# Kernel optimization log

Hardware: AMD Instinct MI355X
Metric: run time of the kernel (lower is better)

The kernel has to match this reference:

```python
import jax, jax.numpy as jnp
import numpy as np

B = 128  # number of graphs/molecules in batch


def setup_inputs() -> dict:
    key = jax.random.key(0)
    ks = jax.random.split(key, 6)
    T, C, D = 131072, 512, 512  # total nodes, feature_dim, out_dim
    hidden_states = jax.random.normal(ks[0], (T, C), dtype=jnp.float32)
    data_batch = jnp.sort(jax.random.randint(ks[1], (T,), 0, B, dtype=jnp.int32))
    lim1 = 1.0 / np.sqrt(C)
    lim2 = 1.0 / np.sqrt(D)
    return {
        "hidden_states": hidden_states,
        "data_batch": data_batch,
        "max_nodes": 1280,
        "ln_gamma": jnp.ones((C,), jnp.float32),
        "ln_beta": jnp.zeros((C,), jnp.float32),
        "W1": jax.random.uniform(ks[2], (D, C), jnp.float32, -lim1, lim1),
        "b1": jax.random.uniform(ks[3], (D,), jnp.float32, -lim1, lim1),
        "W2": jax.random.uniform(ks[4], (D, D), jnp.float32, -lim2, lim2),
        "b2": jax.random.uniform(ks[5], (D,), jnp.float32, -lim2, lim2),
    }


def reference(hidden_states, data_batch, max_nodes, ln_gamma, ln_beta, W1, b1, W2, b2):
    T, C = hidden_states.shape
    # ragged -> dense scatter: position of each node within its batch group
    counts = jnp.bincount(data_batch, length=B)               # [B]
    offsets = jnp.cumsum(counts) - counts                      # exclusive cumsum [B]
    pos = jnp.arange(T, dtype=jnp.int32) - offsets[data_batch]  # [T]
    result = jnp.zeros((B, max_nodes, C), hidden_states.dtype).at[data_batch, pos].set(hidden_states)
    # mask: a padded row is all-zero
    mask = jnp.any(result != 0, axis=-1)[..., None].astype(result.dtype)  # [B, N, 1]
    # LayerNorm (eps=1e-5, torch default)
    mu = jnp.mean(result, axis=-1, keepdims=True)
    var = jnp.mean((result - mu) ** 2, axis=-1, keepdims=True)
    logits = (result - mu) * jax.lax.rsqrt(var + 1e-5) * ln_gamma + ln_beta
    cap_embes = logits @ W1.T + b1                              # [B, N, D]
    features_in = cap_embes @ W2.T + b2                         # [B, N, D]
    features_in = jnp.where(mask == 0, -10000.0, features_in)
    attn = jax.nn.softmax(features_in, axis=1)                  # softmax over nodes
    attn = jnp.where(mask == 0, 0.0, attn)
    return jnp.sum(attn * cap_embes, axis=1)                    # [B, D]
```

## Files before the change

### kernel.cpp

```cpp
#include <hip/hip_runtime.h>
#include <hip/hip_bf16.h>


typedef short short8 __attribute__((ext_vector_type(8)));
typedef short short4v __attribute__((ext_vector_type(4)));
typedef float f32x4 __attribute__((ext_vector_type(4)));

__device__ inline short f2bf(float f) {
    unsigned u = __float_as_uint(f);
    u += 0x7fffu + ((u >> 16) & 1u);
    return (short)(u >> 16);
}

__device__ inline size_t packed_off(int n, int k) {
    const int t = n >> 4, l16n = n & 15;
    const int k0 = k >> 5, quad = (k >> 3) & 3, j = k & 7;
    return ((size_t)((t * 16 + k0) * 64 + quad * 16 + l16n)) * 8 + j;
}

#define PREP_GRID 229

__global__ __launch_bounds__(512)
void esa_prep_all(const float* __restrict__ W1, const float* __restrict__ W2,
                  const float* __restrict__ b1, const float* __restrict__ b2,
                  const int* __restrict__ db, int T, int B,
                  short* __restrict__ W1p, short* __restrict__ W12p,
                  float* __restrict__ b12, int4* __restrict__ entries, int maxent,
                  float* __restrict__ numden) {
    __shared__ int off[513];
    __shared__ int nch[512];
    __shared__ int scan[513];
    const int bid = blockIdx.x;
    const int tid = threadIdx.x;

    if (bid < 64) {
        const int ti = bid >> 3, tj = bid & 7;
        const int wave = tid >> 6;
        const int lane = tid & 63;
        const int quad = lane >> 4;
        const int l16 = lane & 15;
        const int mhalf = wave >> 2;
        const int kq = wave & 3;
        const int kcol = tj * 64 + kq * 16 + l16;

        f32x4 acc[2];
        acc[0] = (f32x4)0.0f; acc[1] = (f32x4)0.0f;
        for (int j0 = 0; j0 < 512; j0 += 32) {
            short8 bfr;
#pragma unroll
            for (int jj = 0; jj < 8; ++jj)
                bfr[jj] = f2bf(W1[(size_t)(j0 + quad * 8 + jj) * 512 + kcol]);
#pragma unroll
            for (int mt = 0; mt < 2; ++mt) {
                const float* ar = W2 + (size_t)(ti * 64 + (mhalf * 2 + mt) * 16 + l16) * 512 +
                                  j0 + quad * 8;
                const float4 a0 = *(const float4*)ar;
                const float4 a1 = *(const float4*)(ar + 4);
                short8 afr = {f2bf(a0.x), f2bf(a0.y), f2bf(a0.z), f2bf(a0.w),
                              f2bf(a1.x), f2bf(a1.y), f2bf(a1.z), f2bf(a1.w)};
                acc[mt] = __builtin_amdgcn_mfma_f32_16x16x32_bf16(afr, bfr,
                                                                  acc[mt], 0, 0, 0);
            }
        }
#pragma unroll
        for (int mt = 0; mt < 2; ++mt)
#pragma unroll
            for (int r = 0; r < 4; ++r) {
                const int n = ti * 64 + (mhalf * 2 + mt) * 16 + quad * 4 + r;
                W12p[packed_off(n, kcol)] = f2bf(acc[mt][r]);
            }
    } else if (bid < 192) {
        const int gid = (bid - 64) * 512 + tid;
        const int i4 = gid * 4;
        const int n = i4 >> 9, k = i4 & 511;
        const float4 a = *(const float4*)(W1 + i4);
        short4v sa = {f2bf(a.x), f2bf(a.y), f2bf(a.z), f2bf(a.w)};
        *(short4v*)(W1p + packed_off(n, k)) = sa;
    } else if (bid < 196) {
        const int row = (bid - 192) * 128 + (tid >> 2);
        const int part = tid & 3;
        const float* wr = W2 + (size_t)row * 512;
        float acc = 0.0f;
#pragma unroll 4
        for (int i = 0; i < 32; ++i) {
            const float4 w = *(const float4*)(wr + (i * 4 + part) * 4);
            const float4 bb = *(const float4*)(b1 + (i * 4 + part) * 4);
            acc += w.x * bb.x + w.y * bb.y + w.z * bb.z + w.w * bb.w;
        }
        acc += __shfl_xor(acc, 1);
        acc += __shfl_xor(acc, 2);
        if (part == 0) b12[row] = acc + b2[row];
    } else if (bid == 196) {
        for (int t = tid; t <= B; t += 512) {
            if (t == B) {
                off[t] = T;
            } else {
                int lo = 0, hi = T;
                while (lo < hi) {
                    int mid = (lo + hi) >> 1;
                    if (db[mid] < t) lo = mid + 1; else hi = mid;
                }
                off[t] = lo;
            }
        }
        __syncthreads();
        for (int t = tid; t < B; t += 512)
            nch[t] = (off[t + 1] - off[t] + 63) >> 6;
        __syncthreads();
        if (tid == 0) {
            int s = 0;
            for (int i = 0; i < B; ++i) { scan[i] = s; s += nch[i]; }
            scan[B] = s;
        }
        __syncthreads();
        for (int t = tid; t < B; t += 512) {
            int cnt = off[t + 1] - off[t];
            for (int j = 0; j < nch[t]; ++j) {
                int v = cnt - j * 64;
                if (v > 64) v = 64;
                entries[scan[t] + j] = make_int4(t, off[t] + j * 64, v, 0);
            }
        }
        int total = scan[B];
        for (int i = total + tid; i < maxent; i += 512)
            entries[i] = make_int4(0, 0, 0, 0);
    } else {
        const int idx = (bid - 197) * 512 + tid;
        float4 z = {0.0f, 0.0f, 0.0f, 0.0f};
        *(float4*)(numden + (size_t)idx * 8) = z;
        *(float4*)(numden + (size_t)idx * 8 + 4) = z;
    }
}

__global__ __launch_bounds__(512, 4)
void esa_fused(const float* __restrict__ x, const float* __restrict__ gamma,
               const float* __restrict__ beta, const short* __restrict__ W1p,
               const short* __restrict__ W12p, const float* __restrict__ b1,
               const float* __restrict__ b12, const int4* __restrict__ entries,
               float* __restrict__ num, float* __restrict__ den) {
    __shared__ short ylds[64 * 512];
    const int4 e = entries[blockIdx.x];
    const int bat = e.x, start = e.y, valid = e.z;
    if (valid <= 0) return;

    const int tid = threadIdx.x;
    const int wave = tid >> 6;
    const int lane = tid & 63;
    const int quad = lane >> 4;
    const int l16 = lane & 15;

    const float4 g0 = *(const float4*)(gamma + lane * 8);
    const float4 g1 = *(const float4*)(gamma + lane * 8 + 4);
    const float4 be0 = *(const float4*)(beta + lane * 8);
    const float4 be1 = *(const float4*)(beta + lane * 8 + 4);

#pragma unroll
    for (int g = 0; g < 2; ++g) {
        float4 ra[4], rb[4];
        float s[4], ss[4];
#pragma unroll
        for (int r = 0; r < 4; ++r) {
            const int m = wave * 8 + g * 4 + r;
            const int mc = m < valid ? m : valid - 1;
            const float* xr = x + (size_t)(start + mc) * 512 + lane * 8;
            ra[r] = *(const float4*)xr;
            rb[r] = *(const float4*)(xr + 4);
        }
#pragma unroll
        for (int r = 0; r < 4; ++r) {
            s[r] = ra[r].x + ra[r].y + ra[r].z + ra[r].w +
                   rb[r].x + rb[r].y + rb[r].z + rb[r].w;
            ss[r] = ra[r].x * ra[r].x + ra[r].y * ra[r].y + ra[r].z * ra[r].z +
                    ra[r].w * ra[r].w + rb[r].x * rb[r].x + rb[r].y * rb[r].y +
                    rb[r].z * rb[r].z + rb[r].w * rb[r].w;
        }
#pragma unroll
        for (int o = 1; o <= 32; o <<= 1) {
#pragma unroll
            for (int r = 0; r < 4; ++r) {
                s[r] += __shfl_xor(s[r], o);
                ss[r] += __shfl_xor(ss[r], o);
            }
        }
#pragma unroll
        for (int r = 0; r < 4; ++r) {
            const int m = wave * 8 + g * 4 + r;
            const float mu = s[r] * (1.0f / 512.0f);
            const float var = ss[r] * (1.0f / 512.0f) - mu * mu;
            const float rstd = rsqrtf(var + 1e-5f);
            short8 outv;
            outv[0] = f2bf((ra[r].x - mu) * rstd * g0.x + be0.x);
            outv[1] = f2bf((ra[r].y - mu) * rstd * g0.y + be0.y);
            outv[2] = f2bf((ra[r].z - mu) * rstd * g0.z + be0.z);
            outv[3] = f2bf((ra[r].w - mu) * rstd * g0.w + be0.w);
            outv[4] = f2bf((rb[r].x - mu) * rstd * g1.x + be1.x);
            outv[5] = f2bf((rb[r].y - mu) * rstd * g1.y + be1.y);
            outv[6] = f2bf((rb[r].z - mu) * rstd * g1.z + be1.z);
            outv[7] = f2bf((rb[r].w - mu) * rstd * g1.w + be1.w);
            *(short8*)&ylds[m * 512 + ((lane ^ (m & 7)) * 8)] = outv;
        }
    }
    __syncthreads();

    const int xr7 = l16 & 7;
    const short* abase = ylds + l16 * 512;
    const bool full = (valid >= 64);

    for (int grp = 0; grp < 2; ++grp) {
        const int n0 = wave * 64 + grp * 32;
        const int ntile0 = n0 >> 4;
        f32x4 acc_c[2][4], acc_f[2][4];
#pragma unroll
        for (int nt = 0; nt < 2; ++nt)
#pragma unroll
            for (int mt = 0; mt < 4; ++mt) {
                acc_c[nt][mt] = (f32x4)0.0f;
                acc_f[nt][mt] = (f32x4)0.0f;
            }
        const short* w1t0 = W1p + (size_t)ntile0 * 8192 + lane * 8;
        const short* w1t1 = w1t0 + 8192;
        const short* w2t0 = W12p + (size_t)ntile0 * 8192 + lane * 8;
        const short* w2t1 = w2t0 + 8192;

        short8 b10 = *(const short8*)(w1t0);
        short8 b11 = *(const short8*)(w1t1);
        short8 b20 = *(const short8*)(w2t0);
        short8 b21 = *(const short8*)(w2t1);

#pragma unroll 2
        for (int k0 = 0; k0 < 16; ++k0) {
            const int kn = (k0 + 1) & 15;
            const short8 nb10 = *(const short8*)(w1t0 + kn * 512);
            const short8 nb11 = *(const short8*)(w1t1 + kn * 512);
            const short8 nb20 = *(const short8*)(w2t0 + kn * 512);
            const short8 nb21 = *(const short8*)(w2t1 + kn * 512);

            const int blk = ((k0 << 2) | quad) ^ xr7;
            const short* ap = abase + blk * 8;

            __builtin_amdgcn_s_setprio(1);
#pragma unroll
            for (int mt = 0; mt < 4; ++mt) {
                const short8 afr = *(const short8*)(ap + mt * 16 * 512);
                acc_c[0][mt] = __builtin_amdgcn_mfma_f32_16x16x32_bf16(
                    afr, b10, acc_c[0][mt], 0, 0, 0);
                acc_c[1][mt] = __builtin_amdgcn_mfma_f32_16x16x32_bf16(
                    afr, b11, acc_c[1][mt], 0, 0, 0);
                acc_f[0][mt] = __builtin_amdgcn_mfma_f32_16x16x32_bf16(
                    afr, b20, acc_f[0][mt], 0, 0, 0);
                acc_f[1][mt] = __builtin_amdgcn_mfma_f32_16x16x32_bf16(
                    afr, b21, acc_f[1][mt], 0, 0, 0);
            }
            __builtin_amdgcn_s_setprio(0);
            b10 = nb10; b11 = nb11; b20 = nb20; b21 = nb21;
        }
#pragma unroll
        for (int nt = 0; nt < 2; ++nt) {
            const int n = n0 + nt * 16 + l16;
            const float bb1 = b1[n];
            const float bb2 = b12[n];
            float se = 0.0f, sec = 0.0f;
            if (full) {
#pragma unroll
                for (int mt = 0; mt < 4; ++mt) {
#pragma unroll
                    for (int r2 = 0; r2 < 4; ++r2) {
                        const float cap = acc_c[nt][mt][r2] + bb1;
                        const float ev = __expf(acc_f[nt][mt][r2] + bb2);
                        se += ev;
                        sec += ev * cap;
                    }
                }
            } else {
#pragma unroll
                for (int mt = 0; mt < 4; ++mt) {
#pragma unroll
                    for (int r2 = 0; r2 < 4; ++r2) {
                        const int m = mt * 16 + quad * 4 + r2;
                        if (m < valid) {
                            const float cap = acc_c[nt][mt][r2] + bb1;
                            const float ev = __expf(acc_f[nt][mt][r2] + bb2);
                            se += ev;
                            sec += ev * cap;
                        }
                    }
                }
            }
            se += __shfl_xor(se, 16);
            se += __shfl_xor(se, 32);
            sec += __shfl_xor(sec, 16);
            sec += __shfl_xor(sec, 32);
            if (quad == 0) atomicAdd(&den[(size_t)bat * 512 + n], se);
            else if (quad == 1) atomicAdd(&num[(size_t)bat * 512 + n], sec);
        }
    }
}

__global__ __launch_bounds__(256)
void esa_finalize(const float* __restrict__ num, const float* __restrict__ den,
                  float* __restrict__ out, int n) {
    const int i = blockIdx.x * 256 + threadIdx.x;
    if (i < n) {
        const float d = den[i];
        out[i] = d > 0.0f ? num[i] / d : 0.0f;
    }
}

extern "C" void kernel_launch(void* const* d_in, const int* in_sizes, int n_in,
                              void* d_out, int out_size, void* d_ws, size_t ws_size,
                              hipStream_t stream) {
    const float* x = (const float*)d_in[0];
    const int* db = (const int*)d_in[1];
    const float* gamma = (const float*)d_in[3];
    const float* beta = (const float*)d_in[4];
    const float* W1 = (const float*)d_in[5];
    const float* b1 = (const float*)d_in[6];
    const float* W2 = (const float*)d_in[7];
    const float* b2 = (const float*)d_in[8];
    float* out = (float*)d_out;

    const int C = in_sizes[3];
    const int D = in_sizes[6];
    const int T = in_sizes[0] / C;
    const int B = out_size / D;
    const int maxent = B + (T + 63) / 64;

    char* ws = (char*)d_ws;
    short* W1p = (short*)(ws);
    short* W12p = (short*)(ws + 524288);
    float* b12 = (float*)(ws + 1048576);
    int4* entries = (int4*)(ws + 1050624);
    size_t numoff = (1050624 + (size_t)maxent * 16 + 255) & ~(size_t)255;
    float* num = (float*)(ws + numoff);
    float* den = (float*)(ws + numoff + (size_t)B * D * 4);

    esa_prep_all<<<PREP_GRID, 512, 0, stream>>>(W1, W2, b1, b2, db, T, B,
                                                W1p, W12p, b12, entries, maxent,
                                                num);
    esa_fused<<<maxent, 512, 0, stream>>>(x, gamma, beta, W1p, W12p, b1, b12,
                                          entries, num, den);
    esa_finalize<<<(B * D + 255) / 256, 256, 0, stream>>>(num, den, out, B * D);
}
```

Before: 469.9 us.

## Shrink row tiles to 48 rows and raise occupancy to six blocks per CU

```diff
diff --git a/kernel.cpp b/kernel.cpp
--- a/kernel.cpp
+++ b/kernel.cpp
@@ -1,6 +1,8 @@
 #include <hip/hip_runtime.h>
 #include <hip/hip_bf16.h>
 
+
+#define ROWS 48
 
 typedef short short8 __attribute__((ext_vector_type(8)));
 typedef short short4v __attribute__((ext_vector_type(4)));
@@ -105,7 +107,7 @@
         }
         __syncthreads();
         for (int t = tid; t < B; t += 512)
-            nch[t] = (off[t + 1] - off[t] + 63) >> 6;
+            nch[t] = (off[t + 1] - off[t] + (ROWS - 1)) / ROWS;
         __syncthreads();
         if (tid == 0) {
             int s = 0;
@@ -116,9 +118,9 @@
         for (int t = tid; t < B; t += 512) {
             int cnt = off[t + 1] - off[t];
             for (int j = 0; j < nch[t]; ++j) {
-                int v = cnt - j * 64;
-                if (v > 64) v = 64;
-                entries[scan[t] + j] = make_int4(t, off[t] + j * 64, v, 0);
+                int v = cnt - j * ROWS;
+                if (v > ROWS) v = ROWS;
+                entries[scan[t] + j] = make_int4(t, off[t] + j * ROWS, v, 0);
             }
         }
         int total = scan[B];
@@ -132,13 +134,13 @@
     }
 }
 
-__global__ __launch_bounds__(512, 4)
+__global__ __launch_bounds__(512, 6)
 void esa_fused(const float* __restrict__ x, const float* __restrict__ gamma,
                const float* __restrict__ beta, const short* __restrict__ W1p,
                const short* __restrict__ W12p, const float* __restrict__ b1,
                const float* __restrict__ b12, const int4* __restrict__ entries,
                float* __restrict__ num, float* __restrict__ den) {
-    __shared__ short ylds[64 * 512];
+    __shared__ short ylds[ROWS * 512];
     const int4 e = entries[blockIdx.x];
     const int bat = e.x, start = e.y, valid = e.z;
     if (valid <= 0) return;
@@ -156,18 +158,18 @@
 
 #pragma unroll
     for (int g = 0; g < 2; ++g) {
-        float4 ra[4], rb[4];
-        float s[4], ss[4];
-#pragma unroll
-        for (int r = 0; r < 4; ++r) {
-            const int m = wave * 8 + g * 4 + r;
+        float4 ra[3], rb[3];
+        float s[3], ss[3];
+#pragma unroll
+        for (int r = 0; r < 3; ++r) {
+            const int m = wave * 6 + g * 3 + r;
             const int mc = m < valid ? m : valid - 1;
-            const float* xr = x + (size_t)(start + mc) * 512 + lane * 8;
-            ra[r] = *(const float4*)xr;
-            rb[r] = *(const float4*)(xr + 4);
-        }
-#pragma unroll
-        for (int r = 0; r < 4; ++r) {
+            const float* xr_ = x + (size_t)(start + mc) * 512 + lane * 8;
+            ra[r] = *(const float4*)xr_;
+            rb[r] = *(const float4*)(xr_ + 4);
+        }
+#pragma unroll
+        for (int r = 0; r < 3; ++r) {
             s[r] = ra[r].x + ra[r].y + ra[r].z + ra[r].w +
                    rb[r].x + rb[r].y + rb[r].z + rb[r].w;
             ss[r] = ra[r].x * ra[r].x + ra[r].y * ra[r].y + ra[r].z * ra[r].z +
@@ -177,14 +179,14 @@
 #pragma unroll
         for (int o = 1; o <= 32; o <<= 1) {
 #pragma unroll
-            for (int r = 0; r < 4; ++r) {
+            for (int r = 0; r < 3; ++r) {
                 s[r] += __shfl_xor(s[r], o);
                 ss[r] += __shfl_xor(ss[r], o);
             }
         }
 #pragma unroll
-        for (int r = 0; r < 4; ++r) {
-            const int m = wave * 8 + g * 4 + r;
+        for (int r = 0; r < 3; ++r) {
+            const int m = wave * 6 + g * 3 + r;
             const float mu = s[r] * (1.0f / 512.0f);
             const float var = ss[r] * (1.0f / 512.0f) - mu * mu;
             const float rstd = rsqrtf(var + 1e-5f);
@@ -204,65 +206,59 @@
 
     const int xr7 = l16 & 7;
     const short* abase = ylds + l16 * 512;
-    const bool full = (valid >= 64);
-
-    for (int grp = 0; grp < 2; ++grp) {
-        const int n0 = wave * 64 + grp * 32;
-        const int ntile0 = n0 >> 4;
-        f32x4 acc_c[2][4], acc_f[2][4];
+    const bool full = (valid >= ROWS);
+
+#pragma unroll 1
+    for (int pass = 0; pass < 2; ++pass) {
+        const int nt0 = pass * 16 + wave * 2;
+        const short* w1a = W1p + (size_t)nt0 * 8192 + lane * 8;
+        const short* w1b = w1a + 8192;
+        const short* w2a = W12p + (size_t)nt0 * 8192 + lane * 8;
+        const short* w2b = w2a + 8192;
+
+        f32x4 acc_c[2][3], acc_f[2][3];
 #pragma unroll
         for (int nt = 0; nt < 2; ++nt)
 #pragma unroll
-            for (int mt = 0; mt < 4; ++mt) {
+            for (int mt = 0; mt < 3; ++mt) {
                 acc_c[nt][mt] = (f32x4)0.0f;
                 acc_f[nt][mt] = (f32x4)0.0f;
             }
-        const short* w1t0 = W1p + (size_t)ntile0 * 8192 + lane * 8;
-        const short* w1t1 = w1t0 + 8192;
-        const short* w2t0 = W12p + (size_t)ntile0 * 8192 + lane * 8;
-        const short* w2t1 = w2t0 + 8192;
-
-        short8 b10 = *(const short8*)(w1t0);
-        short8 b11 = *(const short8*)(w1t1);
-        short8 b20 = *(const short8*)(w2t0);
-        short8 b21 = *(const short8*)(w2t1);
-
-#pragma unroll 2
+
+#pragma unroll 1
         for (int k0 = 0; k0 < 16; ++k0) {
-            const int kn = (k0 + 1) & 15;
-            const short8 nb10 = *(const short8*)(w1t0 + kn * 512);
-            const short8 nb11 = *(const short8*)(w1t1 + kn * 512);
-            const short8 nb20 = *(const short8*)(w2t0 + kn * 512);
-            const short8 nb21 = *(const short8*)(w2t1 + kn * 512);
-
             const int blk = ((k0 << 2) | quad) ^ xr7;
             const short* ap = abase + blk * 8;
-
-            __builtin_amdgcn_s_setprio(1);
-#pragma unroll
-            for (int mt = 0; mt < 4; ++mt) {
-                const short8 afr = *(const short8*)(ap + mt * 16 * 512);
-                acc_c[0][mt] = __builtin_amdgcn_mfma_f32_16x16x32_bf16(
-                    afr, b10, acc_c[0][mt], 0, 0, 0);
-                acc_c[1][mt] = __builtin_amdgcn_mfma_f32_16x16x32_bf16(
-                    afr, b11, acc_c[1][mt], 0, 0, 0);
-                acc_f[0][mt] = __builtin_amdgcn_mfma_f32_16x16x32_bf16(
-                    afr, b20, acc_f[0][mt], 0, 0, 0);
-                acc_f[1][mt] = __builtin_amdgcn_mfma_f32_16x16x32_bf16(
-                    afr, b21, acc_f[1][mt], 0, 0, 0);
-            }
-            __builtin_amdgcn_s_setprio(0);
-            b10 = nb10; b11 = nb11; b20 = nb20; b21 = nb21;
-        }
+            const short8 af0 = *(const short8*)(ap);
+            const short8 af1 = *(const short8*)(ap + 16 * 512);
+            const short8 af2 = *(const short8*)(ap + 32 * 512);
+            const short8 b10 = *(const short8*)(w1a + k0 * 512);
+            const short8 b11 = *(const short8*)(w1b + k0 * 512);
+            const short8 b20 = *(const short8*)(w2a + k0 * 512);
+            const short8 b21 = *(const short8*)(w2b + k0 * 512);
+            acc_c[0][0] = __builtin_amdgcn_mfma_f32_16x16x32_bf16(af0, b10, acc_c[0][0], 0, 0, 0);
+            acc_c[0][1] = __builtin_amdgcn_mfma_f32_16x16x32_bf16(af1, b10, acc_c[0][1], 0, 0, 0);
+            acc_c[0][2] = __builtin_amdgcn_mfma_f32_16x16x32_bf16(af2, b10, acc_c[0][2], 0, 0, 0);
+            acc_c[1][0] = __builtin_amdgcn_mfma_f32_16x16x32_bf16(af0, b11, acc_c[1][0], 0, 0, 0);
+            acc_c[1][1] = __builtin_amdgcn_mfma_f32_16x16x32_bf16(af1, b11, acc_c[1][1], 0, 0, 0);
+            acc_c[1][2] = __builtin_amdgcn_mfma_f32_16x16x32_bf16(af2, b11, acc_c[1][2], 0, 0, 0);
+            acc_f[0][0] = __builtin_amdgcn_mfma_f32_16x16x32_bf16(af0, b20, acc_f[0][0], 0, 0, 0);
+            acc_f[0][1] = __builtin_amdgcn_mfma_f32_16x16x32_bf16(af1, b20, acc_f[0][1], 0, 0, 0);
+            acc_f[0][2] = __builtin_amdgcn_mfma_f32_16x16x32_bf16(af2, b20, acc_f[0][2], 0, 0, 0);
+            acc_f[1][0] = __builtin_amdgcn_mfma_f32_16x16x32_bf16(af0, b21, acc_f[1][0], 0, 0, 0);
+            acc_f[1][1] = __builtin_amdgcn_mfma_f32_16x16x32_bf16(af1, b21, acc_f[1][1], 0, 0, 0);
+            acc_f[1][2] = __builtin_amdgcn_mfma_f32_16x16x32_bf16(af2, b21, acc_f[1][2], 0, 0, 0);
+        }
+
 #pragma unroll
         for (int nt = 0; nt < 2; ++nt) {
-            const int n = n0 + nt * 16 + l16;
+            const int n = pass * 256 + wave * 32 + nt * 16 + l16;
             const float bb1 = b1[n];
             const float bb2 = b12[n];
             float se = 0.0f, sec = 0.0f;
             if (full) {
 #pragma unroll
-                for (int mt = 0; mt < 4; ++mt) {
+                for (int mt = 0; mt < 3; ++mt) {
 #pragma unroll
                     for (int r2 = 0; r2 < 4; ++r2) {
                         const float cap = acc_c[nt][mt][r2] + bb1;
@@ -273,7 +269,7 @@
                 }
             } else {
 #pragma unroll
-                for (int mt = 0; mt < 4; ++mt) {
+                for (int mt = 0; mt < 3; ++mt) {
 #pragma unroll
                     for (int r2 = 0; r2 < 4; ++r2) {
                         const int m = mt * 16 + quad * 4 + r2;
@@ -323,7 +319,7 @@
     const int D = in_sizes[6];
     const int T = in_sizes[0] / C;
     const int B = out_size / D;
-    const int maxent = B + (T + 63) / 64;
+    const int maxent = B + (T + ROWS - 1) / ROWS;
 
     char* ws = (char*)d_ws;
     short* W1p = (short*)(ws);
```

New measurement: 513.9 us. 1.09x slower.
